# Kernel optimization log

Hardware: AMD Instinct MI355X
Metric: run time of the kernel (lower is better)

The kernel has to match this reference:

```python
import jax, jax.numpy as jnp
import numpy as np

N, F, H, FO = 4096, 512, 4, 128  # nodes, in-feat, heads, out-feat per head
NEG_INF = -1e10
LRELU_ALPHA = 0.2


def setup_inputs() -> dict:
    key = jax.random.key(0)
    k_x, k_a, k_w, k_as, k_an = jax.random.split(key, 5)
    X = jax.random.normal(k_x, (N, F), dtype=jnp.float32)
    A = (jax.random.uniform(k_a, (N, N)) < 0.01).astype(jnp.float32)
    A = jnp.minimum(A + jnp.eye(N, dtype=jnp.float32), 1.0)
    W = jax.random.normal(k_w, (H, F, FO), dtype=jnp.float32) * 0.05       # per-head kernels
    b = jnp.zeros((H, FO), dtype=jnp.float32)                               # per-head biases
    a_self = jax.random.normal(k_as, (H, FO), dtype=jnp.float32) * 0.05    # attn_kernel_self (F_,1) per head
    a_neigh = jax.random.normal(k_an, (H, FO), dtype=jnp.float32) * 0.05   # attn_kernel_neigh (F_,1) per head
    return {"X": X, "A": A, "W": W, "b": b, "a_self": a_self, "a_neigh": a_neigh}


def reference(X, A, W, b, a_self, a_neigh):
    # features[h] = X @ W[h] -> [H, N, FO]
    feats = jnp.einsum('nf,hfo->hno', X, W)
    # Nx1 self / neighbor scores per head -> [H, N]
    e_s = jnp.einsum('hno,ho->hn', feats, a_self)
    e_n = jnp.einsum('hno,ho->hn', feats, a_neigh)
    # broadcast-add to [H, N, N], LeakyReLU(0.2), additive adjacency mask
    logits = e_s[:, :, None] + e_n[:, None, :]
    logits = jnp.where(logits > 0, logits, LRELU_ALPHA * logits)
    logits = logits + NEG_INF * (1.0 - A)[None, :, :]
    attn = jax.nn.softmax(logits, axis=-1)          # [H, N, N]
    out = jnp.einsum('hnm,hmo->hno', attn, feats)   # weighted aggregate
    out = out + b[:, None, :]
    # concat heads: [N, H*FO]
    out = jnp.transpose(out, (1, 0, 2)).reshape(X.shape[0], -1)
    return jax.nn.relu(out)
```

## Files before the change

kernel.cpp:

```cpp
#include <hip/hip_runtime.h>
#include <math.h>

#define NODES 4096
#define FIN   512
#define HEADS 4
#define FOUT  128
#define COLS  512
#define MAXNBR 128

typedef _Float16 half8   __attribute__((ext_vector_type(8)));
typedef _Float16 half2v  __attribute__((ext_vector_type(2)));
typedef float    floatx4 __attribute__((ext_vector_type(4)));
typedef float    floatx2 __attribute__((ext_vector_type(2)));
typedef unsigned int uint4v __attribute__((ext_vector_type(4)));

__global__ __launch_bounds__(256) void gemm_scan(
    const float* __restrict__ X, const float* __restrict__ W,
    const float* __restrict__ A,
    const float* __restrict__ a_self, const float* __restrict__ a_neigh,
    _Float16* __restrict__ feats_h, float* __restrict__ ep_s, float* __restrict__ ep_n,
    unsigned int* __restrict__ nbr_pack, int* __restrict__ nbr_cnt)
{
    const int tid = threadIdx.x;

    if (blockIdx.x >= 512) {
        __shared__ int            cnt4[4];
        __shared__ unsigned short idx4[4][MAXNBR];
        const int w = tid >> 6, lane = tid & 63;
        const int row = (blockIdx.x - 512) * 4 + w;
        if (lane == 0) cnt4[w] = 0;
        const uint4v* Arow = (const uint4v*)(A + (size_t)row * NODES);
        for (int q = lane; q < NODES / 4; q += 64) {
            uint4v v = __builtin_nontemporal_load(Arow + q);
            int j = q * 4;
            if (v[0]) { int p = atomicAdd(&cnt4[w], 1); if (p < MAXNBR) idx4[w][p] = (unsigned short)j; }
            if (v[1]) { int p = atomicAdd(&cnt4[w], 1); if (p < MAXNBR) idx4[w][p] = (unsigned short)(j + 1); }
            if (v[2]) { int p = atomicAdd(&cnt4[w], 1); if (p < MAXNBR) idx4[w][p] = (unsigned short)(j + 2); }
            if (v[3]) { int p = atomicAdd(&cnt4[w], 1); if (p < MAXNBR) idx4[w][p] = (unsigned short)(j + 3); }
        }
        __syncthreads();
        unsigned int packed = ((unsigned int)idx4[w][2 * lane + 1] << 16) | idx4[w][2 * lane];
        nbr_pack[(size_t)row * 64 + lane] = packed;
        if (lane == 0) nbr_cnt[row] = min(cnt4[w], MAXNBR);
        return;
    }

    __shared__ _Float16 Ah[2][64][40];
    __shared__ _Float16 Bh[2][64][40];
    __shared__ float red_s[4][64], red_n[4][64];
    const int rowBase = (blockIdx.x >> 3) * 64;
    const int colBase = (blockIdx.x & 7) * 64;
    const int h     = colBase >> 7;
    const int half  = (colBase >> 6) & 1;
    const int obase = colBase & 127;
    const int lane = tid & 63, w = tid >> 6;
    const int quad = lane >> 4, lk = quad * 8, lm = lane & 15;

    const int sr = tid >> 2, sk = (tid & 3) * 8;
    const float* xp = X + (size_t)(rowBase + sr) * FIN + sk;
    const int o = tid & 63, fg = tid >> 6;
    const float* wp = W + ((size_t)h * FIN + fg * 8) * FOUT + obase + o;

    floatx4 acc[4];
    #pragma unroll
    for (int mi = 0; mi < 4; mi++) acc[mi] = (floatx4)0.f;

    float4 xa = *(const float4*)(xp);
    float4 xb = *(const float4*)(xp + 4);
    float rw[8];
    #pragma unroll
    for (int ii = 0; ii < 8; ii++) rw[ii] = wp[(size_t)ii * FOUT];

    for (int it = 0; it < FIN / 32; ++it) {
        const int cur = it & 1;
        half8 ha, hb;
        ha[0] = (_Float16)xa.x; ha[1] = (_Float16)xa.y;
        ha[2] = (_Float16)xa.z; ha[3] = (_Float16)xa.w;
        ha[4] = (_Float16)xb.x; ha[5] = (_Float16)xb.y;
        ha[6] = (_Float16)xb.z; ha[7] = (_Float16)xb.w;
        #pragma unroll
        for (int ii = 0; ii < 8; ii++) hb[ii] = (_Float16)rw[ii];
        *(half8*)&Ah[cur][sr][sk]    = ha;
        *(half8*)&Bh[cur][o][fg * 8] = hb;
        if (it + 1 < FIN / 32) {
            int k0 = (it + 1) * 32;
            xa = *(const float4*)(xp + k0);
            xb = *(const float4*)(xp + k0 + 4);
            #pragma unroll
            for (int ii = 0; ii < 8; ii++) rw[ii] = wp[(size_t)(k0 + ii) * FOUT];
        }
        __syncthreads();
        half8 bfrag = *(const half8*)&Bh[cur][w * 16 + lm][lk];
        #pragma unroll
        for (int mi = 0; mi < 4; mi++) {
            half8 afrag = *(const half8*)&Ah[cur][mi * 16 + lm][lk];
            acc[mi] = __builtin_amdgcn_mfma_f32_16x16x32_f16(afrag, bfrag, acc[mi], 0, 0, 0);
        }
    }

    const int col = colBase + w * 16 + lm;
    const float as = a_self[col], an = a_neigh[col];
    #pragma unroll
    for (int mi = 0; mi < 4; mi++) {
        #pragma unroll
        for (int r = 0; r < 4; r++) {
            int lrow = mi * 16 + quad * 4 + r;
            float v = acc[mi][r];
            feats_h[(size_t)(rowBase + lrow) * COLS + col] = (_Float16)v;
            float vs = v * as, vn = v * an;
            #pragma unroll
            for (int off = 1; off < 16; off <<= 1) {
                vs += __shfl_xor(vs, off, 64);
                vn += __shfl_xor(vn, off, 64);
            }
            if (lm == 0) { red_s[w][lrow] = vs; red_n[w][lrow] = vn; }
        }
    }
    __syncthreads();
    if (tid < 64) {
        float vs = red_s[0][tid] + red_s[1][tid] + red_s[2][tid] + red_s[3][tid];
        float vn = red_n[0][tid] + red_n[1][tid] + red_n[2][tid] + red_n[3][tid];
        size_t slot = (size_t)(half * HEADS + h) * NODES + rowBase + tid;
        ep_s[slot] = vs;
        ep_n[slot] = vn;
    }
}

__global__ __launch_bounds__(256) void aggregate(
    const _Float16* __restrict__ feats_h,
    const float* __restrict__ ep_s, const float* __restrict__ ep_n,
    const unsigned int* __restrict__ nbr_pack, const int* __restrict__ nbr_cnt,
    const float* __restrict__ bias, float* __restrict__ out)
{
    const int i = blockIdx.x;
    const int tid = threadIdx.x;
    const int wv = tid >> 6, lane = tid & 63;
    __shared__ unsigned short s_idx[MAXNBR];
    __shared__ float s_w[HEADS][MAXNBR];

    const int cnt = nbr_cnt[i];
    {
        unsigned v = nbr_pack[(size_t)i * 64 + lane];
        s_idx[2 * lane]     = (unsigned short)(v & 0xFFFF);
        s_idx[2 * lane + 1] = (unsigned short)(v >> 16);
    }

    const float esi = ep_s[wv * NODES + i] + ep_s[(HEADS + wv) * NODES + i];
    const float* en0 = ep_n + wv * NODES;
    const float* en1 = ep_n + (HEADS + wv) * NODES;

    float d = 0.f;
    for (int k = lane; k < cnt; k += 64) {
        int j = s_idx[k];
        float e = esi + en0[j] + en1[j];
        float l = e > 0.f ? e : 0.2f * e;
        float wgt = __expf(l);
        s_w[wv][k] = wgt;
        d += wgt;
    }
    #pragma unroll
    for (int off = 32; off > 0; off >>= 1) d += __shfl_xor(d, off, 64);
    const float dinv = 1.f / d;

    float acc0 = 0.f, acc1 = 0.f;
    const _Float16* fcol = feats_h + wv * FOUT + 2 * lane;
    for (int k0 = 0; k0 < cnt; k0 += 8) {
        int j8[8]; float w8[8];
        #pragma unroll
        for (int u = 0; u < 8; u++) {
            int k = k0 + u;
            bool vld = (k < cnt);
            int kc = vld ? k : k0;
            j8[u] = s_idx[kc];
            w8[u] = vld ? s_w[wv][kc] : 0.f;
        }
        half2v f8[8];
        #pragma unroll
        for (int u = 0; u < 8; u++)
            f8[u] = *(const half2v*)(fcol + (size_t)j8[u] * COLS);
        #pragma unroll
        for (int u = 0; u < 8; u++) {
            acc0 = fmaf(w8[u], (float)f8[u][0], acc0);
            acc1 = fmaf(w8[u], (float)f8[u][1], acc1);
        }
    }

    const int c = wv * FOUT + 2 * lane;
    float o0 = fmaxf(acc0 * dinv + bias[c],     0.f);
    float o1 = fmaxf(acc1 * dinv + bias[c + 1], 0.f);
    floatx2 res; res[0] = o0; res[1] = o1;
    __builtin_nontemporal_store(res, (floatx2*)(out + (size_t)i * COLS + c));
}

extern "C" void kernel_launch(void* const* d_in, const int* in_sizes, int n_in,
                              void* d_out, int out_size, void* d_ws, size_t ws_size,
                              hipStream_t stream) {
    const float* X       = (const float*)d_in[0];
    const float* A       = (const float*)d_in[1];
    const float* W       = (const float*)d_in[2];
    const float* b       = (const float*)d_in[3];
    const float* a_self  = (const float*)d_in[4];
    const float* a_neigh = (const float*)d_in[5];
    float* out = (float*)d_out;

    _Float16*     feats_h  = (_Float16*)d_ws;
    float*        ep_s     = (float*)(feats_h + (size_t)NODES * COLS);
    float*        ep_n     = ep_s + 2 * HEADS * NODES;
    unsigned int* nbr_pack = (unsigned int*)(ep_n + 2 * HEADS * NODES);
    int*          nbr_cnt  = (int*)(nbr_pack + (size_t)NODES * 64);

    gemm_scan<<<1536, 256, 0, stream>>>(X, W, A, a_self, a_neigh,
                                        feats_h, ep_s, ep_n, nbr_pack, nbr_cnt);
    aggregate<<<NODES, 256, 0, stream>>>(feats_h, ep_s, ep_n, nbr_pack, nbr_cnt, b, out);
}
```

Before: 146.6 us.

## Move adjacency scan from GEMM kernel into aggregate kernel

The adjacency row scan that builds the neighbor list moves out of the combined GEMM/scan launch and into the aggregate kernel. Each aggregate block now scans its own row of A with all 256 threads into shared memory. This removes the packed neighbor-list round trip through global memory and lets the GEMM launch run only 512 blocks. The cost is that the 64MB A read now sits on the aggregate kernel's path and no longer overlaps with the GEMM blocks. Neighbor order also changes, since the shared-memory atomics now come from 256 threads rather than one wave.

```diff
diff --git a/kernel.cpp b/kernel.cpp
--- a/kernel.cpp
+++ b/kernel.cpp
@@ -14,36 +14,12 @@
 typedef float    floatx2 __attribute__((ext_vector_type(2)));
 typedef unsigned int uint4v __attribute__((ext_vector_type(4)));
 
-__global__ __launch_bounds__(256) void gemm_scan(
+__global__ __launch_bounds__(256) void gemm_feats(
     const float* __restrict__ X, const float* __restrict__ W,
-    const float* __restrict__ A,
     const float* __restrict__ a_self, const float* __restrict__ a_neigh,
-    _Float16* __restrict__ feats_h, float* __restrict__ ep_s, float* __restrict__ ep_n,
-    unsigned int* __restrict__ nbr_pack, int* __restrict__ nbr_cnt)
+    _Float16* __restrict__ feats_h, float* __restrict__ ep_s, float* __restrict__ ep_n)
 {
     const int tid = threadIdx.x;
-
-    if (blockIdx.x >= 512) {
-        __shared__ int            cnt4[4];
-        __shared__ unsigned short idx4[4][MAXNBR];
-        const int w = tid >> 6, lane = tid & 63;
-        const int row = (blockIdx.x - 512) * 4 + w;
-        if (lane == 0) cnt4[w] = 0;
-        const uint4v* Arow = (const uint4v*)(A + (size_t)row * NODES);
-        for (int q = lane; q < NODES / 4; q += 64) {
-            uint4v v = __builtin_nontemporal_load(Arow + q);
-            int j = q * 4;
-            if (v[0]) { int p = atomicAdd(&cnt4[w], 1); if (p < MAXNBR) idx4[w][p] = (unsigned short)j; }
-            if (v[1]) { int p = atomicAdd(&cnt4[w], 1); if (p < MAXNBR) idx4[w][p] = (unsigned short)(j + 1); }
-            if (v[2]) { int p = atomicAdd(&cnt4[w], 1); if (p < MAXNBR) idx4[w][p] = (unsigned short)(j + 2); }
-            if (v[3]) { int p = atomicAdd(&cnt4[w], 1); if (p < MAXNBR) idx4[w][p] = (unsigned short)(j + 3); }
-        }
-        __syncthreads();
-        unsigned int packed = ((unsigned int)idx4[w][2 * lane + 1] << 16) | idx4[w][2 * lane];
-        nbr_pack[(size_t)row * 64 + lane] = packed;
-        if (lane == 0) nbr_cnt[row] = min(cnt4[w], MAXNBR);
-        return;
-    }
 
     __shared__ _Float16 Ah[2][64][40];
     __shared__ _Float16 Bh[2][64][40];
@@ -127,9 +103,9 @@
 }
 
 __global__ __launch_bounds__(256) void aggregate(
+    const float* __restrict__ A,
     const _Float16* __restrict__ feats_h,
     const float* __restrict__ ep_s, const float* __restrict__ ep_n,
-    const unsigned int* __restrict__ nbr_pack, const int* __restrict__ nbr_cnt,
     const float* __restrict__ bias, float* __restrict__ out)
 {
     const int i = blockIdx.x;
@@ -137,13 +113,24 @@
     const int wv = tid >> 6, lane = tid & 63;
     __shared__ unsigned short s_idx[MAXNBR];
     __shared__ float s_w[HEADS][MAXNBR];
+    __shared__ int s_cnt;
 
-    const int cnt = nbr_cnt[i];
-    {
-        unsigned v = nbr_pack[(size_t)i * 64 + lane];
-        s_idx[2 * lane]     = (unsigned short)(v & 0xFFFF);
-        s_idx[2 * lane + 1] = (unsigned short)(v >> 16);
+    if (tid == 0) s_cnt = 0;
+    __syncthreads();
+
+    const uint4v* Arow = (const uint4v*)(A + (size_t)i * NODES);
+    #pragma unroll
+    for (int q = 0; q < 4; q++) {
+        int idx = q * 256 + tid;
+        uint4v v = __builtin_nontemporal_load(Arow + idx);
+        int j = idx * 4;
+        if (v[0]) { int p = atomicAdd(&s_cnt, 1); if (p < MAXNBR) s_idx[p] = (unsigned short)j; }
+        if (v[1]) { int p = atomicAdd(&s_cnt, 1); if (p < MAXNBR) s_idx[p] = (unsigned short)(j + 1); }
+        if (v[2]) { int p = atomicAdd(&s_cnt, 1); if (p < MAXNBR) s_idx[p] = (unsigned short)(j + 2); }
+        if (v[3]) { int p = atomicAdd(&s_cnt, 1); if (p < MAXNBR) s_idx[p] = (unsigned short)(j + 3); }
     }
+    __syncthreads();
+    const int cnt = min(s_cnt, MAXNBR);
 
     const float esi = ep_s[wv * NODES + i] + ep_s[(HEADS + wv) * NODES + i];
     const float* en0 = ep_n + wv * NODES;
@@ -203,13 +190,10 @@
     const float* a_neigh = (const float*)d_in[5];
     float* out = (float*)d_out;
 
-    _Float16*     feats_h  = (_Float16*)d_ws;
-    float*        ep_s     = (float*)(feats_h + (size_t)NODES * COLS);
-    float*        ep_n     = ep_s + 2 * HEADS * NODES;
-    unsigned int* nbr_pack = (unsigned int*)(ep_n + 2 * HEADS * NODES);
-    int*          nbr_cnt  = (int*)(nbr_pack + (size_t)NODES * 64);
+    _Float16* feats_h = (_Float16*)d_ws;
+    float*    ep_s    = (float*)(feats_h + (size_t)NODES * COLS);
+    float*    ep_n    = ep_s + 2 * HEADS * NODES;
 
-    gemm_scan<<<1536, 256, 0, stream>>>(X, W, A, a_self, a_neigh,
-                                        feats_h, ep_s, ep_n, nbr_pack, nbr_cnt);
-    aggregate<<<NODES, 256, 0, stream>>>(feats_h, ep_s, ep_n, nbr_pack, nbr_cnt, b, out);
+    gemm_feats<<<512, 256, 0, stream>>>(X, W, a_self, a_neigh, feats_h, ep_s, ep_n);
+    aggregate<<<NODES, 256, 0, stream>>>(A, feats_h, ep_s, ep_n, b, out);
 }
```

After: 141.6 us. 3.4% less time.
